# Optimization experiments

Hardware: AMD Instinct MI355X
Metric: run time of the kernel (lower is better)

The kernel has to match this reference:

```python
import jax, jax.numpy as jnp
import numpy as np

N_NODES = 100000
N_EDGES = 3200000
N_FEAT = 512
H_MLP = 256
H_GCN = 256
N_CLS = 40


def setup_inputs() -> dict:
    key = jax.random.key(0)
    ks = jax.random.split(key, 8)
    s = 0.02
    return {
        "x": jax.random.normal(ks[0], (N_NODES, N_FEAT), jnp.float32),
        "edge_index": jax.random.randint(ks[1], (2, N_EDGES), 0, N_NODES, dtype=jnp.int64),
        "W_mlp": jax.random.normal(ks[2], (N_FEAT, H_MLP), jnp.float32) * s,
        "b_mlp": jnp.zeros((H_MLP,), jnp.float32),
        "W1": jax.random.normal(ks[3], (H_MLP, H_GCN), jnp.float32) * s,
        "b1": jnp.zeros((H_GCN,), jnp.float32),
        "W2": jax.random.normal(ks[4], (H_GCN, N_CLS), jnp.float32) * s,
        "b2": jnp.zeros((N_CLS,), jnp.float32),
    }


def _gcn_aggregate(h, row, col, edge_norm, self_coef, n):
    # h: [N, D]; messages along edges col->row with symmetric normalization,
    # plus the self-loop term deg^-1 * h (GCNConv default add_self_loops=True).
    msgs = h[col] * edge_norm[:, None]              # [E, D]
    agg = jax.ops.segment_sum(msgs, row, num_segments=n)
    return agg + h * self_coef[:, None]


def reference(x, edge_index, W_mlp, b_mlp, W1, b1, W2, b2):
    n = x.shape[0]
    row, col = edge_index[0], edge_index[1]
    # degree with self-loops (PyG gcn_norm counts edge weight into col, +1 self-loop)
    deg = jax.ops.segment_sum(jnp.ones(row.shape[0], x.dtype), col, num_segments=n) + 1.0
    dis = jax.lax.rsqrt(deg)                         # deg^-1/2, [N]
    edge_norm = dis[row] * dis[col]                  # [E]
    self_coef = dis * dis                            # deg^-1 for self loops, [N]

    h = jax.nn.relu(x @ W_mlp + b_mlp)               # [N, H_MLP]
    h = _gcn_aggregate(h @ W1, row, col, edge_norm, self_coef, n) + b1
    h = jax.nn.relu(h)
    # dropout is identity in eval mode (F.dropout with training=False)
    out = _gcn_aggregate(h @ W2, row, col, edge_norm, self_coef, n) + b2
    return out
```

## Files before the change

### kernel.cpp

```cpp
#include <hip/hip_runtime.h>

#define NN 100000
#define NE 3200000
#define NF 512
#define NH 256
#define NC 40

#define CH 32768
#define NCH 4
#define NPAD (NCH * CH)
#define PARTS 64
#define SLICE ((NE + PARTS - 1) / PARTS)
#define NBLK ((NN + 255) / 256)

typedef __attribute__((ext_vector_type(8))) short bf16x8;
typedef __attribute__((ext_vector_type(4))) float f32x4;
typedef __attribute__((ext_vector_type(4))) unsigned short u16x4;
typedef __attribute__((ext_vector_type(8))) unsigned short u16x8;

__device__ inline unsigned short f2bf(float f) {
    union { float f; unsigned u; } v; v.f = f;
    unsigned r = v.u + 0x7fffu + ((v.u >> 16) & 1u);
    return (unsigned short)(r >> 16);
}
__device__ inline float bf2f(unsigned short s) {
    union { unsigned u; float f; } v; v.u = ((unsigned)s) << 16;
    return v.f;
}


__global__ __launch_bounds__(512) void hist2_kernel(const int* __restrict__ ei,
                                                    unsigned char* __restrict__ rpart8,
                                                    unsigned char* __restrict__ cpart8) {
    __shared__ unsigned h[CH / 2];
    const int chunk = blockIdx.x, part = blockIdx.y, which = blockIdx.z;
    const int* src = which ? (ei + NE) : ei;
    unsigned char* outp = which ? cpart8 : rpart8;
    const int lo = chunk * CH;
    for (int i = threadIdx.x; i < CH / 2; i += 512) h[i] = 0;
    __syncthreads();
    const int e1 = min((part + 1) * SLICE, NE);
    for (int e = part * SLICE + threadIdx.x; e < e1; e += 512) {
        unsigned v = (unsigned)(src[e] - lo);
        if (v < CH) atomicAdd(&h[v >> 1], 1u << ((v & 1) << 4));
    }
    __syncthreads();
    unsigned char* dst = outp + (size_t)part * NPAD + lo;
    for (int i = threadIdx.x; i < CH; i += 512)
        dst[i] = (unsigned char)((h[i >> 1] >> ((i & 1) << 4)) & 0xffu);
}

__global__ __launch_bounds__(256) void reduce_kernel(const unsigned char* __restrict__ rpart8,
                                                     const unsigned char* __restrict__ cpart8,
                                                     int* __restrict__ row_cnt, float* __restrict__ dis,
                                                     int* __restrict__ bsum) {
    __shared__ int s[256];
    const int tid = threadIdx.x;
    const int v = blockIdx.x * 256 + tid;
    unsigned rs = 0, cs = 0;
    if (v < NN) {
        #pragma unroll 1
        for (int p = 0; p < PARTS; p++) {
            rs += rpart8[(size_t)p * NPAD + v];
            cs += cpart8[(size_t)p * NPAD + v];
        }
        row_cnt[v] = (int)rs;
        dis[v] = rsqrtf((float)cs + 1.0f);
    }
    s[tid] = (int)rs;
    __syncthreads();
    #pragma unroll
    for (int o = 128; o > 0; o >>= 1) {
        if (tid < o) s[tid] += s[tid + o];
        __syncthreads();
    }
    if (tid == 0) bsum[blockIdx.x] = s[0];
}

__global__ __launch_bounds__(512) void scanb_kernel(const int* __restrict__ bsum,
                                                    int* __restrict__ boff) {
    __shared__ int s[512];
    const int t = threadIdx.x;
    int v = (t < NBLK) ? bsum[t] : 0;
    s[t] = v;
    __syncthreads();
    #pragma unroll
    for (int o = 1; o < 512; o <<= 1) {
        int u = (t >= o) ? s[t - o] : 0;
        __syncthreads();
        s[t] += u;
        __syncthreads();
    }
    if (t < NBLK) boff[t] = s[t] - v;
}

__global__ __launch_bounds__(256) void rstart2_kernel(const unsigned char* __restrict__ rpart8,
                                                      const int* __restrict__ row_cnt,
                                                      const int* __restrict__ boff,
                                                      int* __restrict__ row_ptr,
                                                      unsigned* __restrict__ rbase) {
    __shared__ int s[256];
    const int tid = threadIdx.x;
    const int v = blockIdx.x * 256 + tid;
    int cnt = (v < NN) ? row_cnt[v] : 0;
    s[tid] = cnt;
    __syncthreads();
    #pragma unroll
    for (int o = 1; o < 256; o <<= 1) {
        int u = (tid >= o) ? s[tid - o] : 0;
        __syncthreads();
        s[tid] += u;
        __syncthreads();
    }
    if (v < NN) {
        unsigned run = (unsigned)(boff[blockIdx.x] + s[tid] - cnt);
        row_ptr[v] = (int)run;
        #pragma unroll 1
        for (int p = 0; p < PARTS; p++) {
            size_t i = (size_t)p * NPAD + v;
            rbase[i] = run;
            run += rpart8[i];
        }
    }
    if (v == NN) row_ptr[NN] = NE;
}

__global__ __launch_bounds__(512) void fill2d_kernel(const int* __restrict__ ei,
                                                     const unsigned* __restrict__ rbase,
                                                     const float* __restrict__ dis,
                                                     int2* __restrict__ csr) {
    __shared__ unsigned cur[CH / 2];
    const int chunk = blockIdx.x, part = blockIdx.y;
    const int lo = chunk * CH;
    for (int i = threadIdx.x; i < CH / 2; i += 512) cur[i] = 0;
    __syncthreads();
    const unsigned* base = rbase + (size_t)part * NPAD + lo;
    const int e1 = min((part + 1) * SLICE, NE);
    for (int e = part * SLICE + threadIdx.x; e < e1; e += 512) {
        int r = ei[e];
        unsigned rr = (unsigned)(r - lo);
        if (rr < CH) {
            int c = ei[NE + e];
            unsigned sh = (rr & 1) << 4;
            unsigned old = atomicAdd(&cur[rr >> 1], 1u << sh);
            unsigned p = (old >> sh) & 0xffffu;
            unsigned idx = base[rr] + p;
            int2 rec;
            rec.x = c;
            rec.y = __float_as_int(dis[r] * dis[c]);
            csr[idx] = rec;
        }
    }
}

__global__ void wtrans_all(const float* __restrict__ Wm, const float* __restrict__ W1,
                           const float* __restrict__ W2, unsigned short* __restrict__ WTm,
                           unsigned short* __restrict__ W1T, unsigned short* __restrict__ W2T) {
    int t = blockIdx.x * 256 + threadIdx.x;
    if (t < NH * NF) {
        int n = t / NF, k = t % NF;
        WTm[t] = f2bf(Wm[(long)k * NH + n]);
        return;
    }
    t -= NH * NF;
    if (t < NH * NH) {
        int n = t / NH, k = t % NH;
        W1T[t] = f2bf(W1[(long)k * NH + n]);
        return;
    }
    t -= NH * NH;
    if (t < 64 * NH) {
        int n = t / NH, k = t % NH;
        W2T[t] = (n < NC) ? f2bf(W2[(long)k * NC + n]) : (unsigned short)0;
    }
}

template <int BN, bool A_F32, bool BIAS, bool RELU>
__global__ __launch_bounds__(BN == 256 ? 512 : 256)
void gemm_mfma(const void* __restrict__ Ap, const unsigned short* __restrict__ WT,
               const float* __restrict__ bias, unsigned short* __restrict__ C,
               int M, int K) {
    constexpr int BM = 128, BK = 32;
    constexpr int T = (BN == 256) ? 512 : 256;
    constexpr int WN = (BN == 256) ? 2 : 1;
    constexpr int NREP = BN / (WN * 16);
    constexpr int MREP = 2;
    constexpr int ACH = (BM * BK) / 8;
    constexpr int BCH = (BN * BK) / 8;

    __shared__ short As[BM * BK];
    __shared__ short Bs[BN * BK];

    const int tid = threadIdx.x;
    const int lane = tid & 63;
    const int wid = tid >> 6;
    const int wr = wid / WN;
    const int wc = wid % WN;
    const long bm = (long)blockIdx.x * BM;

    f32x4 acc[MREP][NREP];
    #pragma unroll
    for (int i = 0; i < MREP; i++)
        #pragma unroll
        for (int j = 0; j < NREP; j++)
            acc[i][j] = (f32x4){0.f, 0.f, 0.f, 0.f};

    const float* Af = (const float*)Ap;
    const unsigned short* Ab = (const unsigned short*)Ap;

    for (int k0 = 0; k0 < K; k0 += BK) {
        #pragma unroll
        for (int i = 0; i < ACH / T; i++) {
            int ch = tid + i * T;
            int row = ch >> 2, c = ch & 3;
            int sw = c ^ (row & 3) ^ ((row >> 2) & 3);
            long gr = bm + row;
            bf16x8 w;
            if (gr < M) {
                if (A_F32) {
                    float4 v0 = *(const float4*)(Af + gr * K + k0 + c * 8);
                    float4 v1 = *(const float4*)(Af + gr * K + k0 + c * 8 + 4);
                    w[0] = (short)f2bf(v0.x); w[1] = (short)f2bf(v0.y);
                    w[2] = (short)f2bf(v0.z); w[3] = (short)f2bf(v0.w);
                    w[4] = (short)f2bf(v1.x); w[5] = (short)f2bf(v1.y);
                    w[6] = (short)f2bf(v1.z); w[7] = (short)f2bf(v1.w);
                } else {
                    w = *(const bf16x8*)(Ab + gr * K + k0 + c * 8);
                }
            } else {
                w = (bf16x8){0, 0, 0, 0, 0, 0, 0, 0};
            }
            *(bf16x8*)(As + row * BK + sw * 8) = w;
        }
        #pragma unroll
        for (int i = 0; i < BCH / T; i++) {
            int ch = tid + i * T;
            int row = ch >> 2, c = ch & 3;
            int sw = c ^ (row & 3) ^ ((row >> 2) & 3);
            bf16x8 w = *(const bf16x8*)(WT + (long)row * K + k0 + c * 8);
            *(bf16x8*)(Bs + row * BK + sw * 8) = w;
        }
        __syncthreads();

        const int l15 = lane & 15, g = lane >> 4;
        bf16x8 a[MREP];
        #pragma unroll
        for (int mi = 0; mi < MREP; mi++) {
            int row = wr * 32 + mi * 16 + l15;
            int sw = g ^ (row & 3) ^ ((row >> 2) & 3);
            a[mi] = *(const bf16x8*)(As + row * BK + sw * 8);
        }
        #pragma unroll
        for (int ni = 0; ni < NREP; ni++) {
            int row = wc * (NREP * 16) + ni * 16 + l15;
            int sw = g ^ (row & 3) ^ ((row >> 2) & 3);
            bf16x8 b = *(const bf16x8*)(Bs + row * BK + sw * 8);
            #pragma unroll
            for (int mi = 0; mi < MREP; mi++)
                acc[mi][ni] = __builtin_amdgcn_mfma_f32_16x16x32_bf16(a[mi], b, acc[mi][ni], 0, 0, 0);
        }
        __syncthreads();
    }

    const int l15 = lane & 15, l4 = lane >> 4;
    #pragma unroll
    for (int mi = 0; mi < MREP; mi++) {
        long gr0 = bm + wr * 32 + mi * 16 + l4 * 4;
        #pragma unroll
        for (int ni = 0; ni < NREP; ni++) {
            int gc = wc * (NREP * 16) + ni * 16 + l15;
            float bv = BIAS ? bias[gc] : 0.f;
            #pragma unroll
            for (int q = 0; q < 4; q++) {
                long gr = gr0 + q;
                if (gr < M) {
                    float v = acc[mi][ni][q] + bv;
                    if (RELU) v = fmaxf(v, 0.f);
                    C[gr * BN + gc] = f2bf(v);
                }
            }
        }
    }
}

__global__ void agg256_kernel(const unsigned short* __restrict__ t, const int* __restrict__ row_ptr,
                              const int2* __restrict__ csr, const float* __restrict__ dis,
                              const float* __restrict__ bias, unsigned short* __restrict__ out, int n) {
    const int wid = threadIdx.x >> 6, lane = threadIdx.x & 63;
    const int node = blockIdx.x * 4 + wid;
    if (node >= n) return;
    const int half = lane >> 5;
    const int f0 = (lane & 31) * 8;
    const float d = dis[node];
    float a[8];
    if (half == 0) {
        u16x8 sv = *(const u16x8*)(t + (long)node * NH + f0);
        float d2 = d * d;
        #pragma unroll
        for (int j = 0; j < 8; j++) a[j] = bf2f(sv[j]) * d2;
    } else {
        #pragma unroll
        for (int j = 0; j < 8; j++) a[j] = 0.f;
    }
    const int lo = row_ptr[node], hi = row_ptr[node + 1];
    int ee = lo + half;
    for (; ee + 6 < hi; ee += 8) {
        int2 r0 = csr[ee];
        int2 r1 = csr[ee + 2];
        int2 r2 = csr[ee + 4];
        int2 r3 = csr[ee + 6];
        u16x8 v0 = *(const u16x8*)(t + (long)r0.x * NH + f0);
        u16x8 v1 = *(const u16x8*)(t + (long)r1.x * NH + f0);
        u16x8 v2 = *(const u16x8*)(t + (long)r2.x * NH + f0);
        u16x8 v3 = *(const u16x8*)(t + (long)r3.x * NH + f0);
        float w0 = __int_as_float(r0.y), w1 = __int_as_float(r1.y);
        float w2 = __int_as_float(r2.y), w3 = __int_as_float(r3.y);
        #pragma unroll
        for (int j = 0; j < 8; j++)
            a[j] += (bf2f(v0[j]) * w0 + bf2f(v1[j]) * w1) + (bf2f(v2[j]) * w2 + bf2f(v3[j]) * w3);
    }
    for (; ee + 2 < hi; ee += 4) {
        int2 r0 = csr[ee];
        int2 r1 = csr[ee + 2];
        u16x8 v0 = *(const u16x8*)(t + (long)r0.x * NH + f0);
        u16x8 v1 = *(const u16x8*)(t + (long)r1.x * NH + f0);
        float w0 = __int_as_float(r0.y), w1 = __int_as_float(r1.y);
        #pragma unroll
        for (int j = 0; j < 8; j++)
            a[j] += bf2f(v0[j]) * w0 + bf2f(v1[j]) * w1;
    }
    if (ee < hi) {
        int2 r0 = csr[ee];
        u16x8 v0 = *(const u16x8*)(t + (long)r0.x * NH + f0);
        float w0 = __int_as_float(r0.y);
        #pragma unroll
        for (int j = 0; j < 8; j++) a[j] += bf2f(v0[j]) * w0;
    }
    #pragma unroll
    for (int j = 0; j < 8; j++) a[j] += __shfl_xor(a[j], 32);
    if (half == 0) {
        u16x8 o;
        #pragma unroll
        for (int j = 0; j < 8; j++)
            o[j] = f2bf(fmaxf(a[j] + bias[f0 + j], 0.f));
        *(u16x8*)(out + (long)node * NH + f0) = o;
    }
}

__global__ void agg40_kernel(const unsigned short* __restrict__ t, const int* __restrict__ row_ptr,
                             const int2* __restrict__ csr, const float* __restrict__ dis,
                             const float* __restrict__ bias, float* __restrict__ out, int n) {
    const int wid = threadIdx.x >> 6, lane = threadIdx.x & 63;
    const int node = blockIdx.x * 4 + wid;
    if (node >= n) return;
    const int g = lane >> 3;
    const int f0 = (lane & 7) * 8;
    const bool act = f0 < NC;
    const float d = dis[node];
    float a[8];
    #pragma unroll
    for (int j = 0; j < 8; j++) a[j] = 0.f;
    const int lo = row_ptr[node], hi = row_ptr[node + 1];
    if (act) {
        if (g == 0) {
            u16x8 sv = *(const u16x8*)(t + (long)node * 64 + f0);
            float d2 = d * d;
            #pragma unroll
            for (int j = 0; j < 8; j++) a[j] = bf2f(sv[j]) * d2;
        }
        int ee = lo + g;
        for (; ee + 8 < hi; ee += 16) {
            int2 r0 = csr[ee];
            int2 r1 = csr[ee + 8];
            u16x8 v0 = *(const u16x8*)(t + (long)r0.x * 64 + f0);
            u16x8 v1 = *(const u16x8*)(t + (long)r1.x * 64 + f0);
            float w0 = __int_as_float(r0.y), w1 = __int_as_float(r1.y);
            #pragma unroll
            for (int j = 0; j < 8; j++)
                a[j] += bf2f(v0[j]) * w0 + bf2f(v1[j]) * w1;
        }
        if (ee < hi) {
            int2 r0 = csr[ee];
            u16x8 v0 = *(const u16x8*)(t + (long)r0.x * 64 + f0);
            float w0 = __int_as_float(r0.y);
            #pragma unroll
            for (int j = 0; j < 8; j++) a[j] += bf2f(v0[j]) * w0;
        }
    }
    #pragma unroll
    for (int s = 8; s < 64; s <<= 1)
        #pragma unroll
        for (int j = 0; j < 8; j++) a[j] += __shfl_xor(a[j], s);
    if (g == 0 && act) {
        float4 o0, o1;
        o0.x = a[0] + bias[f0 + 0]; o0.y = a[1] + bias[f0 + 1];
        o0.z = a[2] + bias[f0 + 2]; o0.w = a[3] + bias[f0 + 3];
        o1.x = a[4] + bias[f0 + 4]; o1.y = a[5] + bias[f0 + 5];
        o1.z = a[6] + bias[f0 + 6]; o1.w = a[7] + bias[f0 + 7];
        float* dst = out + (long)node * NC + f0;
        *(float4*)dst = o0;
        *(float4*)(dst + 4) = o1;
    }
}


extern "C" void kernel_launch(void* const* d_in, const int* in_sizes, int n_in,
                              void* d_out, int out_size, void* d_ws, size_t ws_size,
                              hipStream_t stream) {
    const float* x     = (const float*)d_in[0];
    const int*   ei    = (const int*)d_in[1];
    const float* W_mlp = (const float*)d_in[2];
    const float* b_mlp = (const float*)d_in[3];
    const float* W1    = (const float*)d_in[4];
    const float* b1    = (const float*)d_in[5];
    const float* W2    = (const float*)d_in[6];
    const float* b2    = (const float*)d_in[7];
    float* out = (float*)d_out;

    float* ws = (float*)d_ws;
    size_t off = 0;
    float*    dis     = ws + off; off += 100096;
    int*      row_cnt = (int*)(ws + off); off += 100096;
    int*      row_ptr = (int*)(ws + off); off += 100096;
    int*      bsum    = (int*)(ws + off); off += 512;
    int*      boff    = (int*)(ws + off); off += 512;
    unsigned char* rpart8 = (unsigned char*)(ws + off); off += (size_t)PARTS * NPAD / 4;
    unsigned char* cpart8 = (unsigned char*)(ws + off); off += (size_t)PARTS * NPAD / 4;
    unsigned* rbase   = (unsigned*)(ws + off); off += (size_t)PARTS * NPAD;
    int2*     csr     = (int2*)(ws + off); off += (size_t)NE * 2;
    unsigned short* WTm = (unsigned short*)(ws + off); off += (NH * NF) / 2;
    unsigned short* W1T = (unsigned short*)(ws + off); off += (NH * NH) / 2;
    unsigned short* W2T = (unsigned short*)(ws + off); off += (64 * NH) / 2;
    unsigned short* h0  = (unsigned short*)(ws + off); off += (size_t)NN * NH / 2;
    unsigned short* t1  = (unsigned short*)(ws + off); off += (size_t)NN * NH / 2;
    unsigned short* t2p = (unsigned short*)(ws + off); off += (size_t)NN * 64 / 2;
    unsigned short* h1  = h0;
    (void)ws_size;

    dim3 gh(NCH, PARTS, 2);
    hist2_kernel<<<gh, 512, 0, stream>>>(ei, rpart8, cpart8);
    reduce_kernel<<<NBLK, 256, 0, stream>>>(rpart8, cpart8, row_cnt, dis, bsum);
    scanb_kernel<<<1, 512, 0, stream>>>(bsum, boff);
    rstart2_kernel<<<NBLK, 256, 0, stream>>>(rpart8, row_cnt, boff, row_ptr, rbase);
    dim3 gf(NCH, PARTS);
    fill2d_kernel<<<gf, 512, 0, stream>>>(ei, rbase, dis, csr);

    wtrans_all<<<(NH * NF + NH * NH + 64 * NH + 255) / 256, 256, 0, stream>>>(
        W_mlp, W1, W2, WTm, W1T, W2T);

    const int mb = (NN + 127) / 128;
    gemm_mfma<256, true, true, true><<<mb, 512, 0, stream>>>(x, WTm, b_mlp, h0, NN, NF);
    gemm_mfma<256, false, false, false><<<mb, 512, 0, stream>>>(h0, W1T, nullptr, t1, NN, NH);
    agg256_kernel<<<(NN + 3) / 4, 256, 0, stream>>>(t1, row_ptr, csr, dis, b1, h1, NN);
    gemm_mfma<64, false, false, false><<<mb, 256, 0, stream>>>(h1, W2T, nullptr, t2p, NN, NH);
    agg40_kernel<<<(NN + 3) / 4, 256, 0, stream>>>(t2p, row_ptr, csr, dis, b2, out, NN);
}
```

Baseline: 595.2 us.

## Fuse MLP and first GCN linear GEMMs via LDS-resident tile; compact t2 stride

Merges the x@W_mlp (bias+ReLU) GEMM and the h0@W1 GEMM into one kernel that keeps each 128-row h0 tile in swizzled shared memory instead of writing and rereading it from global memory. The final 40-class GEMM now stores its output with a 40-column stride instead of 64-column padding, and the aggregation kernel is updated to match. This removes a full intermediate round-trip and shrinks the gathered rows, but the fused kernel uses 80KB of LDS, which limits occupancy to about one block per CU.

```diff
diff --git a/kernel.cpp b/kernel.cpp
--- a/kernel.cpp
+++ b/kernel.cpp
@@ -175,109 +175,213 @@
     }
 }
 
-template <int BN, bool A_F32, bool BIAS, bool RELU>
-__global__ __launch_bounds__(BN == 256 ? 512 : 256)
-void gemm_mfma(const void* __restrict__ Ap, const unsigned short* __restrict__ WT,
-               const float* __restrict__ bias, unsigned short* __restrict__ C,
-               int M, int K) {
-    constexpr int BM = 128, BK = 32;
-    constexpr int T = (BN == 256) ? 512 : 256;
-    constexpr int WN = (BN == 256) ? 2 : 1;
-    constexpr int NREP = BN / (WN * 16);
-    constexpr int MREP = 2;
-    constexpr int ACH = (BM * BK) / 8;
-    constexpr int BCH = (BN * BK) / 8;
-
-    __shared__ short As[BM * BK];
-    __shared__ short Bs[BN * BK];
+__global__ __launch_bounds__(512)
+void gemm12_kernel(const float* __restrict__ x, const unsigned short* __restrict__ WTm,
+                   const float* __restrict__ bmlp, const unsigned short* __restrict__ W1T,
+                   unsigned short* __restrict__ t1, int M) {
+    __shared__ char smem[81920];
+    short* h0s = (short*)smem;
+    short* As  = (short*)smem;
+    short* Bs  = (short*)(smem + 8192);
+    short* Bs2 = (short*)(smem + 65536);
 
     const int tid = threadIdx.x;
     const int lane = tid & 63;
     const int wid = tid >> 6;
-    const int wr = wid / WN;
-    const int wc = wid % WN;
-    const long bm = (long)blockIdx.x * BM;
-
-    f32x4 acc[MREP][NREP];
-    #pragma unroll
-    for (int i = 0; i < MREP; i++)
-        #pragma unroll
-        for (int j = 0; j < NREP; j++)
-            acc[i][j] = (f32x4){0.f, 0.f, 0.f, 0.f};
-
-    const float* Af = (const float*)Ap;
-    const unsigned short* Ab = (const unsigned short*)Ap;
-
-    for (int k0 = 0; k0 < K; k0 += BK) {
-        #pragma unroll
-        for (int i = 0; i < ACH / T; i++) {
-            int ch = tid + i * T;
+    const int wr = wid >> 1;
+    const int wc = wid & 1;
+    const long bm = (long)blockIdx.x * 128;
+    const int l15 = lane & 15, g = lane >> 4, l4 = lane >> 4;
+
+    f32x4 acc[2][8];
+    #pragma unroll
+    for (int i = 0; i < 2; i++)
+        #pragma unroll
+        for (int j = 0; j < 8; j++) acc[i][j] = (f32x4){0.f, 0.f, 0.f, 0.f};
+
+    for (int k0 = 0; k0 < NF; k0 += 32) {
+        {
+            int ch = tid;
             int row = ch >> 2, c = ch & 3;
             int sw = c ^ (row & 3) ^ ((row >> 2) & 3);
             long gr = bm + row;
-            bf16x8 w;
+            bf16x8 w = (bf16x8){0, 0, 0, 0, 0, 0, 0, 0};
             if (gr < M) {
-                if (A_F32) {
-                    float4 v0 = *(const float4*)(Af + gr * K + k0 + c * 8);
-                    float4 v1 = *(const float4*)(Af + gr * K + k0 + c * 8 + 4);
-                    w[0] = (short)f2bf(v0.x); w[1] = (short)f2bf(v0.y);
-                    w[2] = (short)f2bf(v0.z); w[3] = (short)f2bf(v0.w);
-                    w[4] = (short)f2bf(v1.x); w[5] = (short)f2bf(v1.y);
-                    w[6] = (short)f2bf(v1.z); w[7] = (short)f2bf(v1.w);
-                } else {
-                    w = *(const bf16x8*)(Ab + gr * K + k0 + c * 8);
-                }
-            } else {
-                w = (bf16x8){0, 0, 0, 0, 0, 0, 0, 0};
+                float4 v0 = *(const float4*)(x + gr * NF + k0 + c * 8);
+                float4 v1 = *(const float4*)(x + gr * NF + k0 + c * 8 + 4);
+                w[0] = (short)f2bf(v0.x); w[1] = (short)f2bf(v0.y);
+                w[2] = (short)f2bf(v0.z); w[3] = (short)f2bf(v0.w);
+                w[4] = (short)f2bf(v1.x); w[5] = (short)f2bf(v1.y);
+                w[6] = (short)f2bf(v1.z); w[7] = (short)f2bf(v1.w);
             }
-            *(bf16x8*)(As + row * BK + sw * 8) = w;
-        }
-        #pragma unroll
-        for (int i = 0; i < BCH / T; i++) {
-            int ch = tid + i * T;
+            *(bf16x8*)(As + row * 32 + sw * 8) = w;
+        }
+        #pragma unroll
+        for (int i = 0; i < 2; i++) {
+            int ch = tid + i * 512;
             int row = ch >> 2, c = ch & 3;
             int sw = c ^ (row & 3) ^ ((row >> 2) & 3);
-            bf16x8 w = *(const bf16x8*)(WT + (long)row * K + k0 + c * 8);
+            bf16x8 w = *(const bf16x8*)(WTm + (long)row * NF + k0 + c * 8);
+            *(bf16x8*)(Bs + row * 32 + sw * 8) = w;
+        }
+        __syncthreads();
+
+        bf16x8 a[2];
+        #pragma unroll
+        for (int mi = 0; mi < 2; mi++) {
+            int row = wr * 32 + mi * 16 + l15;
+            int sw = g ^ (row & 3) ^ ((row >> 2) & 3);
+            a[mi] = *(const bf16x8*)(As + row * 32 + sw * 8);
+        }
+        #pragma unroll
+        for (int ni = 0; ni < 8; ni++) {
+            int row = wc * 128 + ni * 16 + l15;
+            int sw = g ^ (row & 3) ^ ((row >> 2) & 3);
+            bf16x8 b = *(const bf16x8*)(Bs + row * 32 + sw * 8);
+            #pragma unroll
+            for (int mi = 0; mi < 2; mi++)
+                acc[mi][ni] = __builtin_amdgcn_mfma_f32_16x16x32_bf16(a[mi], b, acc[mi][ni], 0, 0, 0);
+        }
+        __syncthreads();
+    }
+
+    #pragma unroll
+    for (int mi = 0; mi < 2; mi++) {
+        int r0 = wr * 32 + mi * 16 + l4 * 4;
+        #pragma unroll
+        for (int ni = 0; ni < 8; ni++) {
+            int gc = wc * 128 + ni * 16 + l15;
+            float bv = bmlp[gc];
+            int cc = gc >> 3, c7 = gc & 7;
+            #pragma unroll
+            for (int q = 0; q < 4; q++) {
+                int row = r0 + q;
+                float v = fmaxf(acc[mi][ni][q] + bv, 0.f);
+                h0s[row * 256 + ((cc ^ (row & 7)) << 3) + c7] = (short)f2bf(v);
+            }
+        }
+    }
+
+    #pragma unroll
+    for (int i = 0; i < 2; i++)
+        #pragma unroll
+        for (int j = 0; j < 8; j++) acc[i][j] = (f32x4){0.f, 0.f, 0.f, 0.f};
+
+    for (int k2 = 0; k2 < NH; k2 += 32) {
+        #pragma unroll
+        for (int i = 0; i < 2; i++) {
+            int ch = tid + i * 512;
+            int row = ch >> 2, c = ch & 3;
+            int sw = c ^ (row & 3) ^ ((row >> 2) & 3);
+            bf16x8 w = *(const bf16x8*)(W1T + (long)row * NH + k2 + c * 8);
+            *(bf16x8*)(Bs2 + row * 32 + sw * 8) = w;
+        }
+        __syncthreads();
+
+        bf16x8 a[2];
+        #pragma unroll
+        for (int mi = 0; mi < 2; mi++) {
+            int row = wr * 32 + mi * 16 + l15;
+            int cc = (k2 >> 3) + g;
+            a[mi] = *(const bf16x8*)(h0s + row * 256 + ((cc ^ (row & 7)) << 3));
+        }
+        #pragma unroll
+        for (int ni = 0; ni < 8; ni++) {
+            int row = wc * 128 + ni * 16 + l15;
+            int sw = g ^ (row & 3) ^ ((row >> 2) & 3);
+            bf16x8 b = *(const bf16x8*)(Bs2 + row * 32 + sw * 8);
+            #pragma unroll
+            for (int mi = 0; mi < 2; mi++)
+                acc[mi][ni] = __builtin_amdgcn_mfma_f32_16x16x32_bf16(a[mi], b, acc[mi][ni], 0, 0, 0);
+        }
+        __syncthreads();
+    }
+
+    #pragma unroll
+    for (int mi = 0; mi < 2; mi++) {
+        long gr0 = bm + wr * 32 + mi * 16 + l4 * 4;
+        #pragma unroll
+        for (int ni = 0; ni < 8; ni++) {
+            int gc = wc * 128 + ni * 16 + l15;
+            #pragma unroll
+            for (int q = 0; q < 4; q++) {
+                long gr = gr0 + q;
+                if (gr < M) t1[gr * NH + gc] = f2bf(acc[mi][ni][q]);
+            }
+        }
+    }
+}
+
+__global__ __launch_bounds__(256)
+void gemm3_kernel(const unsigned short* __restrict__ A, const unsigned short* __restrict__ W2T,
+                  unsigned short* __restrict__ C, int M) {
+    constexpr int BM = 128, BN = 64, BK = 32;
+    __shared__ short As[BM * BK];
+    __shared__ short Bs[BN * BK];
+
+    const int tid = threadIdx.x;
+    const int lane = tid & 63;
+    const int wid = tid >> 6;
+    const int wr = wid;
+    const long bm = (long)blockIdx.x * BM;
+    const int l15 = lane & 15, g = lane >> 4, l4 = lane >> 4;
+
+    f32x4 acc[2][4];
+    #pragma unroll
+    for (int i = 0; i < 2; i++)
+        #pragma unroll
+        for (int j = 0; j < 4; j++) acc[i][j] = (f32x4){0.f, 0.f, 0.f, 0.f};
+
+    for (int k0 = 0; k0 < NH; k0 += BK) {
+        #pragma unroll
+        for (int i = 0; i < 2; i++) {
+            int ch = tid + i * 256;
+            int row = ch >> 2, c = ch & 3;
+            int sw = c ^ (row & 3) ^ ((row >> 2) & 3);
+            long gr = bm + row;
+            bf16x8 w = (bf16x8){0, 0, 0, 0, 0, 0, 0, 0};
+            if (gr < M) w = *(const bf16x8*)(A + gr * NH + k0 + c * 8);
+            *(bf16x8*)(As + row * BK + sw * 8) = w;
+        }
+        {
+            int ch = tid;
+            int row = ch >> 2, c = ch & 3;
+            int sw = c ^ (row & 3) ^ ((row >> 2) & 3);
+            bf16x8 w = *(const bf16x8*)(W2T + (long)row * NH + k0 + c * 8);
             *(bf16x8*)(Bs + row * BK + sw * 8) = w;
         }
         __syncthreads();
 
-        const int l15 = lane & 15, g = lane >> 4;
-        bf16x8 a[MREP];
-        #pragma unroll
-        for (int mi = 0; mi < MREP; mi++) {
+        bf16x8 a[2];
+        #pragma unroll
+        for (int mi = 0; mi < 2; mi++) {
             int row = wr * 32 + mi * 16 + l15;
             int sw = g ^ (row & 3) ^ ((row >> 2) & 3);
             a[mi] = *(const bf16x8*)(As + row * BK + sw * 8);
         }
         #pragma unroll
-        for (int ni = 0; ni < NREP; ni++) {
-            int row = wc * (NREP * 16) + ni * 16 + l15;
+        for (int ni = 0; ni < 4; ni++) {
+            int row = ni * 16 + l15;
             int sw = g ^ (row & 3) ^ ((row >> 2) & 3);
             bf16x8 b = *(const bf16x8*)(Bs + row * BK + sw * 8);
             #pragma unroll
-            for (int mi = 0; mi < MREP; mi++)
+            for (int mi = 0; mi < 2; mi++)
                 acc[mi][ni] = __builtin_amdgcn_mfma_f32_16x16x32_bf16(a[mi], b, acc[mi][ni], 0, 0, 0);
         }
         __syncthreads();
     }
 
-    const int l15 = lane & 15, l4 = lane >> 4;
-    #pragma unroll
-    for (int mi = 0; mi < MREP; mi++) {
+    #pragma unroll
+    for (int mi = 0; mi < 2; mi++) {
         long gr0 = bm + wr * 32 + mi * 16 + l4 * 4;
         #pragma unroll
-        for (int ni = 0; ni < NREP; ni++) {
-            int gc = wc * (NREP * 16) + ni * 16 + l15;
-            float bv = BIAS ? bias[gc] : 0.f;
+        for (int ni = 0; ni < 4; ni++) {
+            int gc = ni * 16 + l15;
+            if (gc >= NC) continue;
             #pragma unroll
             for (int q = 0; q < 4; q++) {
                 long gr = gr0 + q;
-                if (gr < M) {
-                    float v = acc[mi][ni][q] + bv;
-                    if (RELU) v = fmaxf(v, 0.f);
-                    C[gr * BN + gc] = f2bf(v);
-                }
+                if (gr < M) C[gr * NC + gc] = f2bf(acc[mi][ni][q]);
             }
         }
     }
@@ -363,7 +467,7 @@
     const int lo = row_ptr[node], hi = row_ptr[node + 1];
     if (act) {
         if (g == 0) {
-            u16x8 sv = *(const u16x8*)(t + (long)node * 64 + f0);
+            u16x8 sv = *(const u16x8*)(t + (long)node * NC + f0);
             float d2 = d * d;
             #pragma unroll
             for (int j = 0; j < 8; j++) a[j] = bf2f(sv[j]) * d2;
@@ -372,8 +476,8 @@
         for (; ee + 8 < hi; ee += 16) {
             int2 r0 = csr[ee];
             int2 r1 = csr[ee + 8];
-            u16x8 v0 = *(const u16x8*)(t + (long)r0.x * 64 + f0);
-            u16x8 v1 = *(const u16x8*)(t + (long)r1.x * 64 + f0);
+            u16x8 v0 = *(const u16x8*)(t + (long)r0.x * NC + f0);
+            u16x8 v1 = *(const u16x8*)(t + (long)r1.x * NC + f0);
             float w0 = __int_as_float(r0.y), w1 = __int_as_float(r1.y);
             #pragma unroll
             for (int j = 0; j < 8; j++)
@@ -381,7 +485,7 @@
         }
         if (ee < hi) {
             int2 r0 = csr[ee];
-            u16x8 v0 = *(const u16x8*)(t + (long)r0.x * 64 + f0);
+            u16x8 v0 = *(const u16x8*)(t + (long)r0.x * NC + f0);
             float w0 = __int_as_float(r0.y);
             #pragma unroll
             for (int j = 0; j < 8; j++) a[j] += bf2f(v0[j]) * w0;
@@ -431,10 +535,9 @@
     unsigned short* WTm = (unsigned short*)(ws + off); off += (NH * NF) / 2;
     unsigned short* W1T = (unsigned short*)(ws + off); off += (NH * NH) / 2;
     unsigned short* W2T = (unsigned short*)(ws + off); off += (64 * NH) / 2;
-    unsigned short* h0  = (unsigned short*)(ws + off); off += (size_t)NN * NH / 2;
     unsigned short* t1  = (unsigned short*)(ws + off); off += (size_t)NN * NH / 2;
-    unsigned short* t2p = (unsigned short*)(ws + off); off += (size_t)NN * 64 / 2;
-    unsigned short* h1  = h0;
+    unsigned short* h1  = (unsigned short*)(ws + off); off += (size_t)NN * NH / 2;
+    unsigned short* t2p = (unsigned short*)(ws + off); off += ((size_t)NN * NC + 8) / 2;
     (void)ws_size;
 
     dim3 gh(NCH, PARTS, 2);
@@ -449,9 +552,8 @@
         W_mlp, W1, W2, WTm, W1T, W2T);
 
     const int mb = (NN + 127) / 128;
-    gemm_mfma<256, true, true, true><<<mb, 512, 0, stream>>>(x, WTm, b_mlp, h0, NN, NF);
-    gemm_mfma<256, false, false, false><<<mb, 512, 0, stream>>>(h0, W1T, nullptr, t1, NN, NH);
+    gemm12_kernel<<<mb, 512, 0, stream>>>(x, WTm, b_mlp, W1T, t1, NN);
     agg256_kernel<<<(NN + 3) / 4, 256, 0, stream>>>(t1, row_ptr, csr, dis, b1, h1, NN);
-    gemm_mfma<64, false, false, false><<<mb, 256, 0, stream>>>(h1, W2T, nullptr, t2p, NN, NH);
+    gemm3_kernel<<<mb, 256, 0, stream>>>(h1, W2T, t2p, NN);
     agg40_kernel<<<(NN + 3) / 4, 256, 0, stream>>>(t2p, row_ptr, csr, dis, b2, out, NN);
 }
```

Measured after the change: 582.1 us. 2.2% less time.
